# Performance work log

Hardware: AMD Instinct MI355X
Metric: run time of the kernel (lower is better)

The kernel has to match this reference:

```python
import jax, jax.numpy as jnp
import numpy as np


def setup_inputs() -> dict:
    key = jax.random.key(0)
    k1, k2 = jax.random.split(key)
    B, H = 128, 1024
    log_alpha = jax.random.normal(k1, (B, H), dtype=jnp.float32)
    unnormalized_tran = jax.random.normal(k2, (H, H), dtype=jnp.float32)
    return {"log_alpha": log_alpha, "unnormalized_tran": unnormalized_tran}


def reference(log_alpha, unnormalized_tran):
    # tran[i, j] = log P(state j | state i), rows normalized in log space
    tran = jax.nn.log_softmax(unnormalized_tran, axis=-1)  # (H, H)
    # log-domain matmul: out[b, j] = logsumexp_i(log_alpha[b, i] + tran[i, j])
    # broadcast to (B, H, H) then reduce over the source-state axis i
    out = jax.scipy.special.logsumexp(
        log_alpha[:, :, None] + tran[None, :, :], axis=1
    )  # (B, H)
    return out
```

## Files before the change

kernel.cpp:

```cpp
#include <hip/hip_runtime.h>
#include <hip/hip_bf16.h>
#include <math.h>

#define H 1024
#define B 128
#define PROW 1032

typedef unsigned short u16;
typedef unsigned int u32;
typedef __attribute__((ext_vector_type(8))) short bf16x8;
typedef __attribute__((ext_vector_type(4))) float f32x4;

static __device__ inline u16 f2bf(float x) {
    __hip_bfloat16 h = __float2bfloat16(x);
    return __builtin_bit_cast(u16, h);
}

__global__ __launch_bounds__(256) void k1(const float* __restrict__ U,
                                          u16* __restrict__ expU,
                                          float* __restrict__ invS) {
    const int w = threadIdx.x >> 6, l = threadIdx.x & 63;
    const int r = blockIdx.x * 4 + w;
    const float* Ur = U + (size_t)r * H;
    u16* Er = expU + (size_t)r * H;
    float s = 0.f;
    #pragma unroll
    for (int c = 0; c < 4; ++c) {
        float4 u4 = *reinterpret_cast<const float4*>(Ur + c * 256 + l * 4);
        float e0 = __expf(u4.x), e1 = __expf(u4.y), e2 = __expf(u4.z), e3 = __expf(u4.w);
        s += e0 + e1 + e2 + e3;
        ushort4 o = {f2bf(e0), f2bf(e1), f2bf(e2), f2bf(e3)};
        *reinterpret_cast<ushort4*>(Er + c * 256 + l * 4) = o;
    }
    #pragma unroll
    for (int off = 32; off > 0; off >>= 1) s += __shfl_down(s, off, 64);
    if (l == 0) invS[r] = 1.0f / s;
}

__global__ __launch_bounds__(512) void k2(const float* __restrict__ A,
                                          const u16* __restrict__ expU,
                                          const float* __restrict__ invS,
                                          float* __restrict__ out) {
    __shared__ __align__(16) u16 Pl[16][PROW];
    __shared__ float red[3][2][16][16];

    const int t  = threadIdx.x;
    const int b0 = blockIdx.x * 16;
    const int j0 = blockIdx.y * 32;
    const int l  = t & 63, w = t >> 6;
    const int jh = w & 1, kh = w >> 1;

    {
        const int b  = t >> 5;
        const int kq = (t & 31) * 4;
        #pragma unroll
        for (int pass = 0; pass < 8; ++pass) {
            const int k = kq + pass * 128;
            float4 a4 = *reinterpret_cast<const float4*>(A + (size_t)(b0 + b) * H + k);
            float4 s4 = *reinterpret_cast<const float4*>(invS + k);
            ushort4 o = {f2bf(__expf(a4.x) * s4.x), f2bf(__expf(a4.y) * s4.y),
                         f2bf(__expf(a4.z) * s4.z), f2bf(__expf(a4.w) * s4.w)};
            *reinterpret_cast<ushort4*>(&Pl[b][k]) = o;
        }
    }
    __syncthreads();

    f32x4 acc = {0.f, 0.f, 0.f, 0.f};
    const int col  = j0 + jh * 16 + (l & 15);
    const int krow = (l >> 4) * 8;

    #pragma unroll 2
    for (int s = 0; s < 8; ++s) {
        const int kk = s * 128 + kh * 32 + krow;
        bf16x8 af = *reinterpret_cast<const bf16x8*>(&Pl[l & 15][kk]);
        const u16* bp = expU + (size_t)kk * H + col;
        u32 w0 = (u32)bp[0 * H] | ((u32)bp[1 * H] << 16);
        u32 w1 = (u32)bp[2 * H] | ((u32)bp[3 * H] << 16);
        u32 w2 = (u32)bp[4 * H] | ((u32)bp[5 * H] << 16);
        u32 w3 = (u32)bp[6 * H] | ((u32)bp[7 * H] << 16);
        uint4 bw = {w0, w1, w2, w3};
        bf16x8 bfr = __builtin_bit_cast(bf16x8, bw);
        acc = __builtin_amdgcn_mfma_f32_16x16x32_bf16(af, bfr, acc, 0, 0, 0);
    }

    if (kh != 0) {
        #pragma unroll
        for (int r = 0; r < 4; ++r)
            red[kh - 1][jh][(l >> 4) * 4 + r][l & 15] = acc[r];
    }
    __syncthreads();
    if (kh == 0) {
        #pragma unroll
        for (int r = 0; r < 4; ++r) {
            const int row = (l >> 4) * 4 + r;
            const float v = acc[r] + red[0][jh][row][l & 15]
                                   + red[1][jh][row][l & 15]
                                   + red[2][jh][row][l & 15];
            out[(size_t)(b0 + row) * H + col] = __logf(v);
        }
    }
}

extern "C" void kernel_launch(void* const* d_in, const int* in_sizes, int n_in,
                              void* d_out, int out_size, void* d_ws, size_t ws_size,
                              hipStream_t stream) {
    const float* A = (const float*)d_in[0];
    const float* U = (const float*)d_in[1];
    float* out = (float*)d_out;

    char* ws = (char*)d_ws;
    float* invS = (float*)ws;
    u16* expU   = (u16*)(ws + 4096);

    k1<<<H / 4, 256, 0, stream>>>(U, expU, invS);
    dim3 g(B / 16, H / 32);
    k2<<<g, 512, 0, stream>>>(A, expU, invS, out);
}
```

Measured before the change: 16.25 us.

## Pre-pack normalized transition matrix into MFMA fragment layout and precompute exp(A) in bf16

The first kernel now folds the row normalization into the stored bf16 transition matrix, packed so each group of 8 consecutive k values for one column sits contiguously. It also computes exp(log_alpha) to bf16 in separate blocks of the same launch. The main kernel then loads both MFMA operands with single 16-byte global loads, with no LDS staging of A and no eight strided 2-byte B loads. The reduction now has all four k-groups write to LDS and every thread produce one output. In exchange the prep kernel writes the matrix through an LDS transpose and does more work per block, and the A fragments are read redundantly from global memory by each column block.

New measurement: 14.01 us. -13.8%, faster.

```diff
diff --git a/kernel.cpp b/kernel.cpp
--- a/kernel.cpp
+++ b/kernel.cpp
@@ -1,10 +1,8 @@
 #include <hip/hip_runtime.h>
 #include <hip/hip_bf16.h>
-#include <math.h>
 
 #define H 1024
 #define B 128
-#define PROW 1032
 
 typedef unsigned short u16;
 typedef unsigned int u32;
@@ -16,89 +14,94 @@
     return __builtin_bit_cast(u16, h);
 }
 
-__global__ __launch_bounds__(256) void k1(const float* __restrict__ U,
-                                          u16* __restrict__ expU,
-                                          float* __restrict__ invS) {
-    const int w = threadIdx.x >> 6, l = threadIdx.x & 63;
-    const int r = blockIdx.x * 4 + w;
-    const float* Ur = U + (size_t)r * H;
-    u16* Er = expU + (size_t)r * H;
-    float s = 0.f;
-    #pragma unroll
-    for (int c = 0; c < 4; ++c) {
-        float4 u4 = *reinterpret_cast<const float4*>(Ur + c * 256 + l * 4);
-        float e0 = __expf(u4.x), e1 = __expf(u4.y), e2 = __expf(u4.z), e3 = __expf(u4.w);
-        s += e0 + e1 + e2 + e3;
-        ushort4 o = {f2bf(e0), f2bf(e1), f2bf(e2), f2bf(e3)};
-        *reinterpret_cast<ushort4*>(Er + c * 256 + l * 4) = o;
+__global__ __launch_bounds__(256) void k1(const float* __restrict__ A,
+                                          const float* __restrict__ U,
+                                          u16* __restrict__ expUP,
+                                          u16* __restrict__ expA) {
+    const int t = threadIdx.x, w = t >> 6, l = t & 63;
+    const int blk = blockIdx.x;
+    if (blk < 128) {
+        __shared__ u16 Lq[8][1024];
+        #pragma unroll
+        for (int rr = 0; rr < 2; ++rr) {
+            const int row = w * 2 + rr;
+            const float* Ur = U + (size_t)(blk * 8 + row) * H;
+            float e[16];
+            float s = 0.f;
+            #pragma unroll
+            for (int c = 0; c < 4; ++c) {
+                float4 u4 = *reinterpret_cast<const float4*>(Ur + c * 256 + l * 4);
+                e[c*4+0] = __expf(u4.x); e[c*4+1] = __expf(u4.y);
+                e[c*4+2] = __expf(u4.z); e[c*4+3] = __expf(u4.w);
+                s += e[c*4+0] + e[c*4+1] + e[c*4+2] + e[c*4+3];
+            }
+            #pragma unroll
+            for (int off = 32; off > 0; off >>= 1) s += __shfl_down(s, off, 64);
+            const float is = 1.0f / __shfl(s, 0, 64);
+            #pragma unroll
+            for (int c = 0; c < 4; ++c) {
+                ushort4 o = {f2bf(e[c*4+0]*is), f2bf(e[c*4+1]*is),
+                             f2bf(e[c*4+2]*is), f2bf(e[c*4+3]*is)};
+                *reinterpret_cast<ushort4*>(&Lq[row][c*256 + l*4]) = o;
+            }
+        }
+        __syncthreads();
+        u16* dst = expUP + (size_t)blk * (H * 8);
+        #pragma unroll
+        for (int c = 0; c < 4; ++c) {
+            const int j = c * 256 + t;
+            uint4 v;
+            v.x = (u32)Lq[0][j] | ((u32)Lq[1][j] << 16);
+            v.y = (u32)Lq[2][j] | ((u32)Lq[3][j] << 16);
+            v.z = (u32)Lq[4][j] | ((u32)Lq[5][j] << 16);
+            v.w = (u32)Lq[6][j] | ((u32)Lq[7][j] << 16);
+            *reinterpret_cast<uint4*>(dst + (size_t)j * 8) = v;
+        }
+    } else {
+        const int b = (blk - 128) * 4 + w;
+        const float* Ar = A + (size_t)b * H;
+        u16* Er = expA + (size_t)b * H;
+        #pragma unroll
+        for (int c = 0; c < 4; ++c) {
+            float4 a4 = *reinterpret_cast<const float4*>(Ar + c * 256 + l * 4);
+            ushort4 o = {f2bf(__expf(a4.x)), f2bf(__expf(a4.y)),
+                         f2bf(__expf(a4.z)), f2bf(__expf(a4.w))};
+            *reinterpret_cast<ushort4*>(Er + c * 256 + l * 4) = o;
+        }
     }
-    #pragma unroll
-    for (int off = 32; off > 0; off >>= 1) s += __shfl_down(s, off, 64);
-    if (l == 0) invS[r] = 1.0f / s;
 }
 
-__global__ __launch_bounds__(512) void k2(const float* __restrict__ A,
-                                          const u16* __restrict__ expU,
-                                          const float* __restrict__ invS,
+__global__ __launch_bounds__(512) void k2(const u16* __restrict__ expA,
+                                          const u16* __restrict__ expUP,
                                           float* __restrict__ out) {
-    __shared__ __align__(16) u16 Pl[16][PROW];
-    __shared__ float red[3][2][16][16];
-
-    const int t  = threadIdx.x;
+    __shared__ float red[4][2][4][66];
+    const int t = threadIdx.x, l = t & 63, w = t >> 6;
+    const int jh = w & 1, kh = w >> 1;
     const int b0 = blockIdx.x * 16;
     const int j0 = blockIdx.y * 32;
-    const int l  = t & 63, w = t >> 6;
-    const int jh = w & 1, kh = w >> 1;
+    const int colJ = j0 + jh * 16 + (l & 15);
+    const int arow = b0 + (l & 15);
+    const int kg   = l >> 4;
 
-    {
-        const int b  = t >> 5;
-        const int kq = (t & 31) * 4;
-        #pragma unroll
-        for (int pass = 0; pass < 8; ++pass) {
-            const int k = kq + pass * 128;
-            float4 a4 = *reinterpret_cast<const float4*>(A + (size_t)(b0 + b) * H + k);
-            float4 s4 = *reinterpret_cast<const float4*>(invS + k);
-            ushort4 o = {f2bf(__expf(a4.x) * s4.x), f2bf(__expf(a4.y) * s4.y),
-                         f2bf(__expf(a4.z) * s4.z), f2bf(__expf(a4.w) * s4.w)};
-            *reinterpret_cast<ushort4*>(&Pl[b][k]) = o;
-        }
+    f32x4 acc = {0.f, 0.f, 0.f, 0.f};
+    #pragma unroll
+    for (int s = 0; s < 8; ++s) {
+        const int kk = s * 128 + kh * 32 + kg * 8;
+        bf16x8 af = *reinterpret_cast<const bf16x8*>(expA + (size_t)arow * H + kk);
+        bf16x8 bfv = *reinterpret_cast<const bf16x8*>(expUP + ((size_t)(kk >> 3) * H + colJ) * 8);
+        acc = __builtin_amdgcn_mfma_f32_16x16x32_bf16(af, bfv, acc, 0, 0, 0);
     }
+
+    #pragma unroll
+    for (int r = 0; r < 4; ++r) red[kh][jh][r][l] = acc[r];
     __syncthreads();
 
-    f32x4 acc = {0.f, 0.f, 0.f, 0.f};
-    const int col  = j0 + jh * 16 + (l & 15);
-    const int krow = (l >> 4) * 8;
-
-    #pragma unroll 2
-    for (int s = 0; s < 8; ++s) {
-        const int kk = s * 128 + kh * 32 + krow;
-        bf16x8 af = *reinterpret_cast<const bf16x8*>(&Pl[l & 15][kk]);
-        const u16* bp = expU + (size_t)kk * H + col;
-        u32 w0 = (u32)bp[0 * H] | ((u32)bp[1 * H] << 16);
-        u32 w1 = (u32)bp[2 * H] | ((u32)bp[3 * H] << 16);
-        u32 w2 = (u32)bp[4 * H] | ((u32)bp[5 * H] << 16);
-        u32 w3 = (u32)bp[6 * H] | ((u32)bp[7 * H] << 16);
-        uint4 bw = {w0, w1, w2, w3};
-        bf16x8 bfr = __builtin_bit_cast(bf16x8, bw);
-        acc = __builtin_amdgcn_mfma_f32_16x16x32_bf16(af, bfr, acc, 0, 0, 0);
-    }
-
-    if (kh != 0) {
-        #pragma unroll
-        for (int r = 0; r < 4; ++r)
-            red[kh - 1][jh][(l >> 4) * 4 + r][l & 15] = acc[r];
-    }
-    __syncthreads();
-    if (kh == 0) {
-        #pragma unroll
-        for (int r = 0; r < 4; ++r) {
-            const int row = (l >> 4) * 4 + r;
-            const float v = acc[r] + red[0][jh][row][l & 15]
-                                   + red[1][jh][row][l & 15]
-                                   + red[2][jh][row][l & 15];
-            out[(size_t)(b0 + row) * H + col] = __logf(v);
-        }
-    }
+    const int row = t >> 5, c = t & 31;
+    const int jj = c >> 4, cc = c & 15;
+    const int ll = (row >> 2) * 16 + cc, r = row & 3;
+    const float v = red[0][jj][r][ll] + red[1][jj][r][ll]
+                  + red[2][jj][r][ll] + red[3][jj][r][ll];
+    out[(size_t)(b0 + row) * H + j0 + c] = __logf(v);
 }
 
 extern "C" void kernel_launch(void* const* d_in, const int* in_sizes, int n_in,
@@ -109,10 +112,10 @@
     float* out = (float*)d_out;
 
     char* ws = (char*)d_ws;
-    float* invS = (float*)ws;
-    u16* expU   = (u16*)(ws + 4096);
+    u16* expUP = (u16*)ws;
+    u16* expA  = (u16*)(ws + (size_t)2 * 1024 * 1024);
 
-    k1<<<H / 4, 256, 0, stream>>>(U, expU, invS);
+    k1<<<160, 256, 0, stream>>>(A, U, expUP, expA);
     dim3 g(B / 16, H / 32);
-    k2<<<g, 512, 0, stream>>>(A, expU, invS, out);
+    k2<<<g, 512, 0, stream>>>(expA, expUP, out);
 }
```
